# Performance work log

Measured on AMD Instinct MI355X. Metric: run time of the kernel, lower is better.

The kernel has to match this reference:

```python
import jax, jax.numpy as jnp
import numpy as np

EMBED_DIM = 256
B, H, S = 8, 20, 1024


def setup_inputs() -> dict:
    key = jax.random.key(0)
    ks = jax.random.split(key, 10)
    E = EMBED_DIM
    d2, d4 = 2 * E, 4 * E

    def lin(kw, kb, out_dim, in_dim):
        bound = 1.0 / np.sqrt(in_dim)
        w = jax.random.uniform(kw, (out_dim, in_dim), minval=-bound, maxval=bound, dtype=jnp.float32)
        b = jax.random.uniform(kb, (out_dim,), minval=-bound, maxval=bound, dtype=jnp.float32)
        return w, b

    wc_w, wc_b = lin(ks[0], ks[1], d2, d2)
    wh_w, wh_b = lin(ks[2], ks[3], d2, d2)
    qt_w, qt_b = lin(ks[4], ks[5], 1, d2)
    wf_w, wf_b = lin(ks[6], ks[7], E, d4)

    hist = jax.random.normal(ks[8], (B, H, S, d2), dtype=jnp.float32)
    cur = jax.random.normal(ks[9], (B, S, d2), dtype=jnp.float32)
    return {
        "wca_history_embeddings": hist,
        "wca_current_embeddings": cur,
        "wc_w": wc_w, "wc_b": wc_b,
        "wh_w": wh_w, "wh_b": wh_b,
        "qt_w": qt_w, "qt_b": qt_b,
        "wf_w": wf_w, "wf_b": wf_b,
    }


def reference(wca_history_embeddings, wca_current_embeddings,
              wc_w, wc_b, wh_w, wh_b, qt_w, qt_b, wf_w, wf_b):
    # hist: [B, H, S, 2E]; cur: [B, S, 2E]
    c_proj = jnp.einsum('bsd,ed->bse', wca_current_embeddings, wc_w) + wc_b   # [B,S,2E]
    h_proj = jnp.einsum('bhsd,ed->bhse', wca_history_embeddings, wh_w) + wh_b  # [B,H,S,2E]
    gate = jax.nn.sigmoid(c_proj[:, None, :, :] + h_proj)                      # [B,H,S,2E]
    # alpha[b,h,s] = qt(gate) -- raw scores, NO softmax (matches original)
    alpha = jnp.einsum('bhse,e->bhs', gate, qt_w[0]) + qt_b[0]                 # [B,H,S]
    # weighted neighbor sum over history dim
    summed = jnp.einsum('bhs,bhsd->bsd', alpha, wca_history_embeddings)        # [B,S,2E]
    fused = jnp.concatenate([wca_current_embeddings, summed], axis=-1)         # [B,S,4E]
    final = jnp.einsum('bsd,ed->bse', fused, wf_w) + wf_b                      # [B,S,E]
    return final
```

## Files before the change

### kernel.cpp

```cpp
#include <hip/hip_runtime.h>
#include <hip/hip_bf16.h>
#include <stdint.h>

static constexpr int Bn = 8, Hn = 20, Sn = 1024, En = 256, D2 = 512, D4 = 1024;
static constexpr int Mall = Bn * Hn * Sn;
static constexpr int BS   = Bn * Sn;

typedef __attribute__((ext_vector_type(8))) short bf16x8;
typedef __attribute__((ext_vector_type(4))) float f32x4;

__device__ __forceinline__ unsigned short f2bf(float f) {
  unsigned int u = __float_as_uint(f);
  u += 0x7FFFu + ((u >> 16) & 1u);
  return (unsigned short)(u >> 16);
}
__device__ __forceinline__ float bf2f(unsigned short u) {
  return __uint_as_float(((unsigned int)u) << 16);
}
__device__ __forceinline__ float sigmoid_fast(float x) {
  return __builtin_amdgcn_rcpf(1.0f + __expf(-x));
}
__device__ __forceinline__ unsigned int packbf_trunc(float a, float b) {
  return __builtin_amdgcn_perm(__float_as_uint(b), __float_as_uint(a),
                               0x07060302u);
}
__device__ __forceinline__ unsigned int packbf_rne(float a, float b) {
  return ((unsigned int)f2bf(b) << 16) | (unsigned int)f2bf(a);
}
__device__ __forceinline__ uint4 pack8_trunc(float4 f0, float4 f1) {
  uint4 p;
  p.x = packbf_trunc(f0.x, f0.y);
  p.y = packbf_trunc(f0.z, f0.w);
  p.z = packbf_trunc(f1.x, f1.y);
  p.w = packbf_trunc(f1.z, f1.w);
  return p;
}

typedef const __attribute__((address_space(1))) void gv_t;
typedef __attribute__((address_space(3))) void lv_t;
__device__ __forceinline__ void gload_lds16(const void* g, void* l) {
  __builtin_amdgcn_global_load_lds((gv_t*)g, (lv_t*)l, 16, 0, 0);
}

__global__ __launch_bounds__(256) void k_convert_weights(
    const float* __restrict__ wc, const float* __restrict__ wh,
    const float* __restrict__ wf,
    unsigned short* __restrict__ wcb, unsigned short* __restrict__ whb,
    unsigned short* __restrict__ wfb) {
  int idx4 = blockIdx.x * 256 + threadIdx.x;
  int a = idx4 >> 16;
  int r = idx4 & 65535;
  const float* s = (a == 0) ? wc : (a == 1) ? wh : wf;
  unsigned short* d = (a == 0) ? wcb : (a == 1) ? whb : wfb;
  float4 v = reinterpret_cast<const float4*>(s)[r];
  ushort4 o;
  o.x = f2bf(v.x); o.y = f2bf(v.y); o.z = f2bf(v.z); o.w = f2bf(v.w);
  reinterpret_cast<ushort4*>(d)[r] = o;
}

template <int MODE>
__global__ __launch_bounds__(256) void k_gemm_bt(
    const float* __restrict__ A,
    const unsigned short* __restrict__ Bw,
    const float* __restrict__ bias,
    const unsigned short* __restrict__ cproj,
    const float* __restrict__ qtw,
    const float* __restrict__ qtb,
    unsigned short* __restrict__ cproj_out,
    float* __restrict__ alpha_out) {
  __shared__ __align__(16) unsigned char ldsA[128 * 128];
  __shared__ __align__(16) unsigned char ldsB[128 * 128];

  const int tid = threadIdx.x;
  const int lane = tid & 63, wave = tid >> 6;
  const int lrow = lane & 15, lk = lane >> 4;
  const int row0 = blockIdx.x * 128;
  const f32x4 zero4 = {0.f, 0.f, 0.f, 0.f};

  float asum[2][4];
  if (MODE == 1) {
#pragma unroll
    for (int rf = 0; rf < 2; ++rf)
#pragma unroll
      for (int r = 0; r < 4; ++r) asum[rf][r] = 0.f;
  }

  const int nc_begin = (MODE == 0) ? blockIdx.y : 0;
  const int nc_end   = (MODE == 0) ? (int)blockIdx.y + 1 : 4;

  for (int nc = nc_begin; nc < nc_end; ++nc) {
    f32x4 acc[2][8];
#pragma unroll
    for (int rf = 0; rf < 2; ++rf)
#pragma unroll
      for (int cf = 0; cf < 8; ++cf) acc[rf][cf] = zero4;

    for (int kt = 0; kt < 8; ++kt) {
      __syncthreads();
#pragma unroll
      for (int slot = 0; slot < 4; ++slot) {
        int idx = (slot * 256 + tid) * 8;
        int row = idx >> 6, k = idx & 63;
        const float* src = A + (size_t)(row0 + row) * 512 + kt * 64 + k;
        float4 f0 = *reinterpret_cast<const float4*>(src);
        float4 f1 = *reinterpret_cast<const float4*>(src + 4);
        uint4 p = pack8_trunc(f0, f1);
        int off = row * 128 + ((k * 2) ^ ((row & 7) << 4));
        *reinterpret_cast<uint4*>(ldsA + off) = p;
      }
#pragma unroll
      for (int c = 0; c < 4; ++c) {
        int ci = c * 256 + tid;
        int n = ci >> 3, kc = (ci & 7) * 8;
        const unsigned short* src =
            Bw + (size_t)(nc * 128 + n) * 512 + kt * 64 + kc;
        uint4 p = *reinterpret_cast<const uint4*>(src);
        int off = n * 128 + ((kc * 2) ^ ((n & 7) << 4));
        *reinterpret_cast<uint4*>(ldsB + off) = p;
      }
      __syncthreads();
#pragma unroll
      for (int ks = 0; ks < 2; ++ks) {
        int kbyte = ks * 64 + lk * 16;
        bf16x8 af[2];
#pragma unroll
        for (int rf = 0; rf < 2; ++rf) {
          int ar = wave * 32 + rf * 16 + lrow;
          af[rf] = *reinterpret_cast<const bf16x8*>(
              ldsA + ar * 128 + (kbyte ^ ((ar & 7) << 4)));
        }
#pragma unroll
        for (int cf = 0; cf < 8; ++cf) {
          int br = cf * 16 + lrow;
          bf16x8 bf = *reinterpret_cast<const bf16x8*>(
              ldsB + br * 128 + (kbyte ^ ((br & 7) << 4)));
#pragma unroll
          for (int rf = 0; rf < 2; ++rf)
            acc[rf][cf] = __builtin_amdgcn_mfma_f32_16x16x32_bf16(
                af[rf], bf, acc[rf][cf], 0, 0, 0);
        }
      }
    }

    if (MODE == 0) {
#pragma unroll
      for (int cf = 0; cf < 8; ++cf) {
        int e = nc * 128 + cf * 16 + lrow;
        float bse = bias[e];
#pragma unroll
        for (int rf = 0; rf < 2; ++rf)
#pragma unroll
          for (int r = 0; r < 4; ++r) {
            int row = row0 + wave * 32 + rf * 16 + lk * 4 + r;
            cproj_out[(size_t)row * 512 + e] = f2bf(acc[rf][cf][r] + bse);
          }
      }
    } else {
#pragma unroll
      for (int cf = 0; cf < 8; ++cf) {
        int e = nc * 128 + cf * 16 + lrow;
        float whb = bias[e];
        float qw = qtw[e];
#pragma unroll
        for (int rf = 0; rf < 2; ++rf)
#pragma unroll
          for (int r = 0; r < 4; ++r) {
            int row = row0 + wave * 32 + rf * 16 + lk * 4 + r;
            int bsrow = ((row / (Hn * Sn)) << 10) | (row & 1023);
            float cp = bf2f(cproj[(size_t)bsrow * 512 + e]);
            float g = sigmoid_fast(acc[rf][cf][r] + whb + cp);
            asum[rf][r] = fmaf(g, qw, asum[rf][r]);
          }
      }
    }
  }

  if (MODE == 1) {
#pragma unroll
    for (int off = 1; off < 16; off <<= 1) {
#pragma unroll
      for (int rf = 0; rf < 2; ++rf)
#pragma unroll
        for (int r = 0; r < 4; ++r)
          asum[rf][r] += __shfl_xor(asum[rf][r], off, 64);
    }
    if (lrow == 0) {
      float qb = qtb[0];
#pragma unroll
      for (int rf = 0; rf < 2; ++rf)
#pragma unroll
        for (int r = 0; r < 4; ++r) {
          int row = row0 + wave * 32 + rf * 16 + lk * 4 + r;
          alpha_out[row] = asum[rf][r] + qb;
        }
    }
  }
}

__global__ __launch_bounds__(512, 2) void k_alpha_summed(
    const float* __restrict__ A,
    const unsigned short* __restrict__ Bw,
    const float* __restrict__ bias,
    const unsigned short* __restrict__ cproj,
    const float* __restrict__ qtw,
    const float* __restrict__ qtb,
    unsigned short* __restrict__ summed) {
  __shared__ __align__(16) unsigned char ldsA[81920];
  __shared__ __align__(16) unsigned char ldsB[65536];
  __shared__ __align__(16) unsigned char ldsC[4096];

  const int tid = threadIdx.x;
  const int lane = tid & 63, wave = tid >> 6;
  const int lrow = lane & 15, lk = lane >> 4;
  const int wc = wave;
  const int b = blockIdx.x >> 8;
  const int s0 = (blockIdx.x & 255) * 4;
  const size_t rowbase = (size_t)b * 20480;
  const f32x4 zero4 = {0.f, 0.f, 0.f, 0.f};

  const unsigned short* gB0 =
      Bw + (size_t)(wave * 64 + (lane >> 2)) * 512 +
      ((lane & 3) ^ ((lane >> 3) & 3)) * 8;

  auto issueB = [&](int k) {
#pragma unroll
    for (int j = 0; j < 4; ++j)
      gload_lds16(gB0 + (size_t)j * 8192 + k * 32,
                  (char*)ldsB + (k & 1) * 32768 + wave * 4096 + j * 1024);
  };

  float4 pa0[5], pa1[5];
  auto issueA = [&](int bt, float4 (&pa)[5]) {
#pragma unroll
    for (int j = 0; j < 5; ++j) {
      int u = (bt * 5 + j) * 512 + tid;
      int mr = u >> 7, c4 = u & 127;
      pa[j] = *reinterpret_cast<const float4*>(
          A + (rowbase + (size_t)(mr >> 2) * 1024 + s0 + (mr & 3)) * 512 +
          c4 * 4);
    }
  };
  auto writeA = [&](int bt, float4 (&pa)[5]) {
#pragma unroll
    for (int j = 0; j < 5; ++j) {
      int u = (bt * 5 + j) * 512 + tid;
      int mr = u >> 7, c4 = u & 127;
      unsigned int u0 = packbf_rne(pa[j].x, pa[j].y);
      unsigned int u1 = packbf_rne(pa[j].z, pa[j].w);
      int off = mr * 1024 + (((c4 >> 1) ^ (mr & 7)) << 4) + ((c4 & 1) << 3);
      *reinterpret_cast<uint2*>(ldsA + off) = make_uint2(u0, u1);
    }
  };

  if (wave < 4) {
    const unsigned short* csrc = cproj + ((size_t)b * 1024 + s0) * 512;
    gload_lds16(csrc + tid * 8, (char*)ldsC + wave * 1024);
  }
  issueA(0, pa0);
  issueA(1, pa1);
  writeA(0, pa0);
  issueA(2, pa0);
  writeA(1, pa1);
  issueA(3, pa1);
  writeA(2, pa0);
  writeA(3, pa1);
  issueB(0);
  issueB(1);
  __syncthreads();

  f32x4 acc[5][4];
#pragma unroll
  for (int tm = 0; tm < 5; ++tm)
#pragma unroll
    for (int n = 0; n < 4; ++n) acc[tm][n] = zero4;

#pragma unroll 4
  for (int k = 0; k < 16; ++k) {
    bf16x8 af[5];
#pragma unroll
    for (int tm = 0; tm < 5; ++tm) {
      int r = tm * 16 + lrow;
      int g = (k * 4 + lk) ^ (r & 7);
      af[tm] = *reinterpret_cast<const bf16x8*>(ldsA + r * 1024 + g * 16);
    }
    const unsigned char* bbase = ldsB + (k & 1) * 32768 + wave * 4096;
#pragma unroll
    for (int n = 0; n < 4; ++n) {
      int rl = n * 16 + lrow;
      int slot = lk ^ ((rl >> 1) & 3);
      bf16x8 bv = *reinterpret_cast<const bf16x8*>(bbase + rl * 64 + slot * 16);
#pragma unroll
      for (int tm = 0; tm < 5; ++tm)
        acc[tm][n] = __builtin_amdgcn_mfma_f32_16x16x32_bf16(af[tm], bv,
                                                             acc[tm][n], 0, 0,
                                                             0);
    }
    asm volatile("s_waitcnt lgkmcnt(0)" ::: "memory");
    __builtin_amdgcn_sched_barrier(0);
    if (k < 14) {
      issueB(k + 2);
      __builtin_amdgcn_sched_barrier(0);
      asm volatile("s_waitcnt vmcnt(4)" ::: "memory");
    } else if (k == 14) {
      asm volatile("s_waitcnt vmcnt(0)" ::: "memory");
    }
    __builtin_amdgcn_sched_barrier(0);
  }

  float asum[5][4];
#pragma unroll
  for (int tm = 0; tm < 5; ++tm)
#pragma unroll
    for (int r = 0; r < 4; ++r) asum[tm][r] = 0.f;

  const unsigned short* cpl = reinterpret_cast<const unsigned short*>(ldsC);
#pragma unroll
  for (int n = 0; n < 4; ++n) {
    int e = wc * 64 + n * 16 + lrow;
    float whb = bias[e];
    float qw = qtw[e];
    float cpv[4];
#pragma unroll
    for (int si = 0; si < 4; ++si) cpv[si] = bf2f(cpl[si * 512 + e]);
#pragma unroll
    for (int tm = 0; tm < 5; ++tm)
#pragma unroll
      for (int r = 0; r < 4; ++r) {
        float g = sigmoid_fast(acc[tm][n][r] + whb + cpv[r]);
        asum[tm][r] = fmaf(g, qw, asum[tm][r]);
      }
  }
#pragma unroll
  for (int off = 1; off < 16; off <<= 1)
#pragma unroll
    for (int tm = 0; tm < 5; ++tm)
#pragma unroll
      for (int r = 0; r < 4; ++r)
        asum[tm][r] += __shfl_xor(asum[tm][r], off, 64);

  __syncthreads();
  float* red = reinterpret_cast<float*>(ldsB);
  if (lrow == 0) {
#pragma unroll
    for (int tm = 0; tm < 5; ++tm)
#pragma unroll
      for (int r = 0; r < 4; ++r)
        red[wc * 80 + tm * 16 + lk * 4 + r] = asum[tm][r];
  }
  __syncthreads();

  if (wave < 4) {
    const int si = wave;
    const float qb = qtb[0];
    float o[8];
#pragma unroll
    for (int j = 0; j < 8; ++j) o[j] = 0.f;
#pragma unroll
    for (int h = 0; h < 20; ++h) {
      int mr = h * 4 + si;
      float a = qb;
#pragma unroll
      for (int wq = 0; wq < 8; ++wq) a += red[wq * 80 + mr];
      int g = lane ^ (mr & 7);
      bf16x8 av = *reinterpret_cast<const bf16x8*>(ldsA + mr * 1024 + g * 16);
#pragma unroll
      for (int j = 0; j < 8; ++j)
        o[j] = fmaf(a, bf2f((unsigned short)av[j]), o[j]);
    }
    uint4 pk;
    pk.x = packbf_rne(o[0], o[1]);
    pk.y = packbf_rne(o[2], o[3]);
    pk.z = packbf_rne(o[4], o[5]);
    pk.w = packbf_rne(o[6], o[7]);
    size_t orow = (size_t)b * 1024 + s0 + si;
    reinterpret_cast<uint4*>(summed)[orow * 64 + lane] = pk;
  }
}

__global__ __launch_bounds__(256) void k_summed(
    const float* __restrict__ hist, const float* __restrict__ alpha,
    unsigned short* __restrict__ summed) {
  int idx = blockIdx.x * 256 + threadIdx.x;
  int bs = idx >> 7, c4 = idx & 127;
  int b = bs >> 10, s = bs & 1023;
  const float4* hp = reinterpret_cast<const float4*>(hist);
  float4 acc = make_float4(0.f, 0.f, 0.f, 0.f);
#pragma unroll
  for (int h = 0; h < Hn; ++h) {
    int bh = b * Hn + h;
    float a = alpha[(bh << 10) + s];
    float4 v = hp[(size_t)(bh * 1024 + s) * 128 + c4];
    acc.x = fmaf(a, v.x, acc.x);
    acc.y = fmaf(a, v.y, acc.y);
    acc.z = fmaf(a, v.z, acc.z);
    acc.w = fmaf(a, v.w, acc.w);
  }
  ushort4 o;
  o.x = f2bf(acc.x); o.y = f2bf(acc.y); o.z = f2bf(acc.z); o.w = f2bf(acc.w);
  reinterpret_cast<ushort4*>(summed)[idx] = o;
}

__global__ __launch_bounds__(256) void k_final(
    const float* __restrict__ cur,
    const unsigned short* __restrict__ summed,
    const unsigned short* __restrict__ wfb16,
    const float* __restrict__ wf_bias,
    float* __restrict__ out) {
  __shared__ __align__(16) unsigned char ldsA[64 * 128];
  __shared__ __align__(16) unsigned char ldsB[128 * 128];
  const int tid = threadIdx.x;
  const int lane = tid & 63, wave = tid >> 6;
  const int lrow = lane & 15, lk = lane >> 4;
  const int row0 = blockIdx.x * 64;
  const int n0 = blockIdx.y * 128;
  const f32x4 zero4 = {0.f, 0.f, 0.f, 0.f};

  f32x4 acc[8];
#pragma unroll
  for (int cf = 0; cf < 8; ++cf) acc[cf] = zero4;

  for (int kt = 0; kt < 16; ++kt) {
    __syncthreads();
#pragma unroll
    for (int slot = 0; slot < 2; ++slot) {
      int idx = (slot * 256 + tid) * 8;
      int row = idx >> 6, k = idx & 63;
      int gcol = kt * 64 + k;
      uint4 p;
      if (kt < 8) {
        const float* src = cur + (size_t)(row0 + row) * 512 + gcol;
        float4 f0 = *reinterpret_cast<const float4*>(src);
        float4 f1 = *reinterpret_cast<const float4*>(src + 4);
        p = pack8_trunc(f0, f1);
      } else {
        p = *reinterpret_cast<const uint4*>(
            summed + (size_t)(row0 + row) * 512 + gcol - 512);
      }
      int off = row * 128 + ((k * 2) ^ ((row & 7) << 4));
      *reinterpret_cast<uint4*>(ldsA + off) = p;
    }
#pragma unroll
    for (int c = 0; c < 4; ++c) {
      int ci = c * 256 + tid;
      int n = ci >> 3, kc = (ci & 7) * 8;
      uint4 p = *reinterpret_cast<const uint4*>(
          wfb16 + (size_t)(n0 + n) * 1024 + kt * 64 + kc);
      int off = n * 128 + ((kc * 2) ^ ((n & 7) << 4));
      *reinterpret_cast<uint4*>(ldsB + off) = p;
    }
    __syncthreads();
#pragma unroll
    for (int ks = 0; ks < 2; ++ks) {
      int kbyte = ks * 64 + lk * 16;
      int ar = wave * 16 + lrow;
      bf16x8 a = *reinterpret_cast<const bf16x8*>(
          ldsA + ar * 128 + (kbyte ^ ((ar & 7) << 4)));
#pragma unroll
      for (int cf = 0; cf < 8; ++cf) {
        int br = cf * 16 + lrow;
        bf16x8 b = *reinterpret_cast<const bf16x8*>(
            ldsB + br * 128 + (kbyte ^ ((br & 7) << 4)));
        acc[cf] = __builtin_amdgcn_mfma_f32_16x16x32_bf16(a, b, acc[cf], 0, 0, 0);
      }
    }
  }
#pragma unroll
  for (int cf = 0; cf < 8; ++cf) {
    int col = n0 + cf * 16 + lrow;
    float bse = wf_bias[col];
#pragma unroll
    for (int r = 0; r < 4; ++r) {
      int row = row0 + wave * 16 + lk * 4 + r;
      out[(size_t)row * 256 + col] = acc[cf][r] + bse;
    }
  }
}

extern "C" void kernel_launch(void* const* d_in, const int* in_sizes, int n_in,
                              void* d_out, int out_size, void* d_ws,
                              size_t ws_size, hipStream_t stream) {
  (void)in_sizes; (void)n_in; (void)out_size;
  const float* hist = (const float*)d_in[0];
  const float* cur  = (const float*)d_in[1];
  const float* wc_w = (const float*)d_in[2];
  const float* wc_b = (const float*)d_in[3];
  const float* wh_w = (const float*)d_in[4];
  const float* wh_b = (const float*)d_in[5];
  const float* qt_w = (const float*)d_in[6];
  const float* qt_b = (const float*)d_in[7];
  const float* wf_w = (const float*)d_in[8];
  const float* wf_b = (const float*)d_in[9];
  float* out = (float*)d_out;
  char* ws = (char*)d_ws;

  unsigned short* wcb    = (unsigned short*)(ws);
  unsigned short* whb    = (unsigned short*)(ws + 524288);
  unsigned short* wfb    = (unsigned short*)(ws + 1048576);
  unsigned short* cproj  = (unsigned short*)(ws + 1572864);
  float*          alpha  = (float*)(ws + 9961472);
  unsigned short* summed = (unsigned short*)(ws + 10616832);
  const size_t NEED = 19005440;

  k_convert_weights<<<dim3(768), dim3(256), 0, stream>>>(wc_w, wh_w, wf_w, wcb,
                                                         whb, wfb);
  k_gemm_bt<0><<<dim3(BS / 128, 4), dim3(256), 0, stream>>>(
      cur, wcb, wc_b, nullptr, nullptr, nullptr, cproj, nullptr);
  if (ws_size >= NEED) {
    k_alpha_summed<<<dim3(2048), dim3(512), 0, stream>>>(
        hist, whb, wh_b, cproj, qt_w, qt_b, summed);
  } else {
    k_gemm_bt<1><<<dim3(Mall / 128, 1), dim3(256), 0, stream>>>(
        hist, whb, wh_b, cproj, qt_w, qt_b, nullptr, alpha);
    k_summed<<<dim3(4096), dim3(256), 0, stream>>>(hist, alpha, summed);
  }
  k_final<<<dim3(BS / 64, 2), dim3(256), 0, stream>>>(cur, summed, wfb, wf_b,
                                                      out);
}
```

Baseline: 223.0 us.

## Halve per-block sequence tile in fused alpha kernel to raise occupancy

Each block of the fused alpha/summed kernel now covers 2 sequence positions (40 history rows, padded to 3 M-tiles) instead of 4. This shrinks LDS use and raises the launch-bounds occupancy target, and the grid grows to 4096 blocks. The c_proj staging buffer is dropped in favour of direct global loads. B-weight loading changes from double-buffered async prefetch to a single buffer guarded by __syncthreads each k-step. The aim is more resident blocks to hide memory latency, but each weight tile is now reloaded for half as many rows, padding wastes some MFMA work, and load/compute overlap is reduced.

New measurement: 257.0 us. +15.3%, slower.

```diff
diff --git a/kernel.cpp b/kernel.cpp
--- a/kernel.cpp
+++ b/kernel.cpp
@@ -197,7 +197,7 @@
   }
 }
 
-__global__ __launch_bounds__(512, 2) void k_alpha_summed(
+__global__ __launch_bounds__(512, 4) void k_alpha_summed(
     const float* __restrict__ A,
     const unsigned short* __restrict__ Bw,
     const float* __restrict__ bias,
@@ -205,28 +205,26 @@
     const float* __restrict__ qtw,
     const float* __restrict__ qtb,
     unsigned short* __restrict__ summed) {
-  __shared__ __align__(16) unsigned char ldsA[81920];
-  __shared__ __align__(16) unsigned char ldsB[65536];
-  __shared__ __align__(16) unsigned char ldsC[4096];
+  __shared__ __align__(16) unsigned char ldsA[49152];
+  __shared__ __align__(16) unsigned char ldsB[32768];
 
   const int tid = threadIdx.x;
   const int lane = tid & 63, wave = tid >> 6;
   const int lrow = lane & 15, lk = lane >> 4;
   const int wc = wave;
-  const int b = blockIdx.x >> 8;
-  const int s0 = (blockIdx.x & 255) * 4;
+  const int b = blockIdx.x >> 9;
+  const int s0 = (blockIdx.x & 511) * 2;
   const size_t rowbase = (size_t)b * 20480;
   const f32x4 zero4 = {0.f, 0.f, 0.f, 0.f};
 
   const unsigned short* gB0 =
-      Bw + (size_t)(wave * 64 + (lane >> 2)) * 512 +
-      ((lane & 3) ^ ((lane >> 3) & 3)) * 8;
-
+      Bw + (size_t)(lane >> 2) * 512 + ((lane & 3) ^ ((lane >> 3) & 3)) * 8;
   auto issueB = [&](int k) {
 #pragma unroll
-    for (int j = 0; j < 4; ++j)
-      gload_lds16(gB0 + (size_t)j * 8192 + k * 32,
-                  (char*)ldsB + (k & 1) * 32768 + wave * 4096 + j * 1024);
+    for (int j = 0; j < 4; ++j) {
+      int W = j * 8 + wave;
+      gload_lds16(gB0 + (size_t)W * 8192 + k * 32, (char*)ldsB + W * 1024);
+    }
   };
 
   float4 pa0[5], pa1[5];
@@ -236,7 +234,7 @@
       int u = (bt * 5 + j) * 512 + tid;
       int mr = u >> 7, c4 = u & 127;
       pa[j] = *reinterpret_cast<const float4*>(
-          A + (rowbase + (size_t)(mr >> 2) * 1024 + s0 + (mr & 3)) * 512 +
+          A + (rowbase + (size_t)(mr >> 1) * 1024 + s0 + (mr & 1)) * 512 +
           c4 * 4);
     }
   };
@@ -245,111 +243,93 @@
     for (int j = 0; j < 5; ++j) {
       int u = (bt * 5 + j) * 512 + tid;
       int mr = u >> 7, c4 = u & 127;
-      unsigned int u0 = packbf_rne(pa[j].x, pa[j].y);
-      unsigned int u1 = packbf_rne(pa[j].z, pa[j].w);
       int off = mr * 1024 + (((c4 >> 1) ^ (mr & 7)) << 4) + ((c4 & 1) << 3);
-      *reinterpret_cast<uint2*>(ldsA + off) = make_uint2(u0, u1);
+      *reinterpret_cast<uint2*>(ldsA + off) =
+          make_uint2(packbf_rne(pa[j].x, pa[j].y),
+                     packbf_rne(pa[j].z, pa[j].w));
     }
   };
 
-  if (wave < 4) {
-    const unsigned short* csrc = cproj + ((size_t)b * 1024 + s0) * 512;
-    gload_lds16(csrc + tid * 8, (char*)ldsC + wave * 1024);
-  }
   issueA(0, pa0);
   issueA(1, pa1);
   writeA(0, pa0);
-  issueA(2, pa0);
   writeA(1, pa1);
-  issueA(3, pa1);
-  writeA(2, pa0);
-  writeA(3, pa1);
   issueB(0);
-  issueB(1);
   __syncthreads();
 
-  f32x4 acc[5][4];
-#pragma unroll
-  for (int tm = 0; tm < 5; ++tm)
+  f32x4 acc[3][4];
+#pragma unroll
+  for (int tm = 0; tm < 3; ++tm)
 #pragma unroll
     for (int n = 0; n < 4; ++n) acc[tm][n] = zero4;
 
-#pragma unroll 4
   for (int k = 0; k < 16; ++k) {
-    bf16x8 af[5];
-#pragma unroll
-    for (int tm = 0; tm < 5; ++tm) {
+    bf16x8 af[3];
+#pragma unroll
+    for (int tm = 0; tm < 3; ++tm) {
       int r = tm * 16 + lrow;
       int g = (k * 4 + lk) ^ (r & 7);
       af[tm] = *reinterpret_cast<const bf16x8*>(ldsA + r * 1024 + g * 16);
     }
-    const unsigned char* bbase = ldsB + (k & 1) * 32768 + wave * 4096;
 #pragma unroll
     for (int n = 0; n < 4; ++n) {
-      int rl = n * 16 + lrow;
+      int rl = wc * 64 + n * 16 + lrow;
       int slot = lk ^ ((rl >> 1) & 3);
-      bf16x8 bv = *reinterpret_cast<const bf16x8*>(bbase + rl * 64 + slot * 16);
-#pragma unroll
-      for (int tm = 0; tm < 5; ++tm)
+      bf16x8 bv = *reinterpret_cast<const bf16x8*>(ldsB + rl * 64 + slot * 16);
+#pragma unroll
+      for (int tm = 0; tm < 3; ++tm)
         acc[tm][n] = __builtin_amdgcn_mfma_f32_16x16x32_bf16(af[tm], bv,
                                                              acc[tm][n], 0, 0,
                                                              0);
     }
-    asm volatile("s_waitcnt lgkmcnt(0)" ::: "memory");
-    __builtin_amdgcn_sched_barrier(0);
-    if (k < 14) {
-      issueB(k + 2);
-      __builtin_amdgcn_sched_barrier(0);
-      asm volatile("s_waitcnt vmcnt(4)" ::: "memory");
-    } else if (k == 14) {
-      asm volatile("s_waitcnt vmcnt(0)" ::: "memory");
-    }
-    __builtin_amdgcn_sched_barrier(0);
-  }
-
-  float asum[5][4];
-#pragma unroll
-  for (int tm = 0; tm < 5; ++tm)
+    __syncthreads();
+    if (k < 15) {
+      issueB(k + 1);
+      __syncthreads();
+    }
+  }
+
+  float asum[3][4];
+#pragma unroll
+  for (int tm = 0; tm < 3; ++tm)
 #pragma unroll
     for (int r = 0; r < 4; ++r) asum[tm][r] = 0.f;
 
-  const unsigned short* cpl = reinterpret_cast<const unsigned short*>(ldsC);
+  const size_t cpbase = ((size_t)b * 1024 + s0) * 512;
 #pragma unroll
   for (int n = 0; n < 4; ++n) {
     int e = wc * 64 + n * 16 + lrow;
     float whb = bias[e];
     float qw = qtw[e];
-    float cpv[4];
-#pragma unroll
-    for (int si = 0; si < 4; ++si) cpv[si] = bf2f(cpl[si * 512 + e]);
-#pragma unroll
-    for (int tm = 0; tm < 5; ++tm)
+    float cp0 = bf2f(cproj[cpbase + e]);
+    float cp1 = bf2f(cproj[cpbase + 512 + e]);
+#pragma unroll
+    for (int tm = 0; tm < 3; ++tm)
 #pragma unroll
       for (int r = 0; r < 4; ++r) {
-        float g = sigmoid_fast(acc[tm][n][r] + whb + cpv[r]);
+        float g = sigmoid_fast(acc[tm][n][r] + whb + ((r & 1) ? cp1 : cp0));
         asum[tm][r] = fmaf(g, qw, asum[tm][r]);
       }
   }
 #pragma unroll
   for (int off = 1; off < 16; off <<= 1)
 #pragma unroll
-    for (int tm = 0; tm < 5; ++tm)
+    for (int tm = 0; tm < 3; ++tm)
 #pragma unroll
       for (int r = 0; r < 4; ++r)
         asum[tm][r] += __shfl_xor(asum[tm][r], off, 64);
 
-  __syncthreads();
   float* red = reinterpret_cast<float*>(ldsB);
   if (lrow == 0) {
 #pragma unroll
-    for (int tm = 0; tm < 5; ++tm)
+    for (int tm = 0; tm < 3; ++tm)
 #pragma unroll
       for (int r = 0; r < 4; ++r)
-        red[wc * 80 + tm * 16 + lk * 4 + r] = asum[tm][r];
+        red[wc * 48 + tm * 16 + lk * 4 + r] = asum[tm][r];
   }
   __syncthreads();
 
-  if (wave < 4) {
+  if (wave < 2) {
     const int si = wave;
     const float qb = qtb[0];
     float o[8];
@@ -357,10 +337,10 @@
     for (int j = 0; j < 8; ++j) o[j] = 0.f;
 #pragma unroll
     for (int h = 0; h < 20; ++h) {
-      int mr = h * 4 + si;
+      int mr = h * 2 + si;
       float a = qb;
 #pragma unroll
-      for (int wq = 0; wq < 8; ++wq) a += red[wq * 80 + mr];
+      for (int w = 0; w < 8; ++w) a += red[w * 48 + mr];
       int g = lane ^ (mr & 7);
       bf16x8 av = *reinterpret_cast<const bf16x8*>(ldsA + mr * 1024 + g * 16);
 #pragma unroll
@@ -506,7 +486,7 @@
   k_gemm_bt<0><<<dim3(BS / 128, 4), dim3(256), 0, stream>>>(
       cur, wcb, wc_b, nullptr, nullptr, nullptr, cproj, nullptr);
   if (ws_size >= NEED) {
-    k_alpha_summed<<<dim3(2048), dim3(512), 0, stream>>>(
+    k_alpha_summed<<<dim3(4096), dim3(512), 0, stream>>>(
         hist, whb, wh_b, cproj, qt_w, qt_b, summed);
   } else {
     k_gemm_bt<1><<<dim3(Mall / 128, 1), dim3(256), 0, stream>>>(
```

## Load weight fragments directly into registers instead of staging through LDS

Applied to the files above, without the earlier changes.

In the fused alpha/summed kernel, the weight (B) operand is now read straight from global memory into registers with a three-deep register prefetch ring, in place of the double-buffered LDS staging with explicit waitcnt barriers. This removes 64KB of LDS per block and the LDS write/read traffic for B. The K loop is fully unrolled through a macro, and the reduction buffer moves to a small dedicated LDS array, which also drops one __syncthreads. The trade-offs are higher register pressure from the prefetch ring and global load latency that is now hidden only by a short prefetch distance.

Result: slower. 260.9 us (+17.0%).

```diff
diff --git a/kernel.cpp b/kernel.cpp
--- a/kernel.cpp
+++ b/kernel.cpp
@@ -206,8 +206,8 @@
     const float* __restrict__ qtb,
     unsigned short* __restrict__ summed) {
   __shared__ __align__(16) unsigned char ldsA[81920];
-  __shared__ __align__(16) unsigned char ldsB[65536];
   __shared__ __align__(16) unsigned char ldsC[4096];
+  __shared__ float ldsR[8 * 80];
 
   const int tid = threadIdx.x;
   const int lane = tid & 63, wave = tid >> 6;
@@ -218,15 +218,17 @@
   const size_t rowbase = (size_t)b * 20480;
   const f32x4 zero4 = {0.f, 0.f, 0.f, 0.f};
 
-  const unsigned short* gB0 =
-      Bw + (size_t)(wave * 64 + (lane >> 2)) * 512 +
-      ((lane & 3) ^ ((lane >> 3) & 3)) * 8;
-
-  auto issueB = [&](int k) {
-#pragma unroll
-    for (int j = 0; j < 4; ++j)
-      gload_lds16(gB0 + (size_t)j * 8192 + k * 32,
-                  (char*)ldsB + (k & 1) * 32768 + wave * 4096 + j * 1024);
+  const char* gB = reinterpret_cast<const char*>(Bw);
+  int boff[4];
+#pragma unroll
+  for (int n = 0; n < 4; ++n)
+    boff[n] = ((wc * 64 + n * 16 + lrow) << 10) + (lk << 4);
+
+  bf16x8 bv0[4], bv1[4], bv2[4];
+  auto loadB = [&](int K, bf16x8 (&bv)[4]) {
+#pragma unroll
+    for (int n = 0; n < 4; ++n)
+      bv[n] = *reinterpret_cast<const bf16x8*>(gB + boff[n] + K * 64);
   };
 
   float4 pa0[5], pa1[5];
@@ -264,8 +266,6 @@
   issueA(3, pa1);
   writeA(2, pa0);
   writeA(3, pa1);
-  issueB(0);
-  issueB(1);
   __syncthreads();
 
   f32x4 acc[5][4];
@@ -274,38 +274,33 @@
 #pragma unroll
     for (int n = 0; n < 4; ++n) acc[tm][n] = zero4;
 
-#pragma unroll 4
-  for (int k = 0; k < 16; ++k) {
-    bf16x8 af[5];
-#pragma unroll
-    for (int tm = 0; tm < 5; ++tm) {
-      int r = tm * 16 + lrow;
-      int g = (k * 4 + lk) ^ (r & 7);
-      af[tm] = *reinterpret_cast<const bf16x8*>(ldsA + r * 1024 + g * 16);
-    }
-    const unsigned char* bbase = ldsB + (k & 1) * 32768 + wave * 4096;
-#pragma unroll
-    for (int n = 0; n < 4; ++n) {
-      int rl = n * 16 + lrow;
-      int slot = lk ^ ((rl >> 1) & 3);
-      bf16x8 bv = *reinterpret_cast<const bf16x8*>(bbase + rl * 64 + slot * 16);
-#pragma unroll
-      for (int tm = 0; tm < 5; ++tm)
-        acc[tm][n] = __builtin_amdgcn_mfma_f32_16x16x32_bf16(af[tm], bv,
-                                                             acc[tm][n], 0, 0,
-                                                             0);
-    }
-    asm volatile("s_waitcnt lgkmcnt(0)" ::: "memory");
-    __builtin_amdgcn_sched_barrier(0);
-    if (k < 14) {
-      issueB(k + 2);
-      __builtin_amdgcn_sched_barrier(0);
-      asm volatile("s_waitcnt vmcnt(4)" ::: "memory");
-    } else if (k == 14) {
-      asm volatile("s_waitcnt vmcnt(0)" ::: "memory");
-    }
-    __builtin_amdgcn_sched_barrier(0);
-  }
+  loadB(0, bv0);
+  loadB(1, bv1);
+  loadB(2, bv2);
+
+#define KSTEP(K, BV)                                                       \
+  {                                                                        \
+    bf16x8 af[5];                                                          \
+    _Pragma("unroll") for (int tm = 0; tm < 5; ++tm) {                     \
+      int r = tm * 16 + lrow;                                              \
+      int g = ((K) * 4 + lk) ^ (r & 7);                                    \
+      af[tm] =                                                             \
+          *reinterpret_cast<const bf16x8*>(ldsA + r * 1024 + g * 16);      \
+    }                                                                      \
+    _Pragma("unroll") for (int n = 0; n < 4; ++n)                          \
+        _Pragma("unroll") for (int tm = 0; tm < 5; ++tm) acc[tm][n] =      \
+        __builtin_amdgcn_mfma_f32_16x16x32_bf16(af[tm], BV[n],             \
+                                                acc[tm][n], 0, 0, 0);      \
+    if ((K) < 13) loadB((K) + 3, BV);                                      \
+  }
+
+  KSTEP(0, bv0)  KSTEP(1, bv1)  KSTEP(2, bv2)
+  KSTEP(3, bv0)  KSTEP(4, bv1)  KSTEP(5, bv2)
+  KSTEP(6, bv0)  KSTEP(7, bv1)  KSTEP(8, bv2)
+  KSTEP(9, bv0)  KSTEP(10, bv1) KSTEP(11, bv2)
+  KSTEP(12, bv0) KSTEP(13, bv1) KSTEP(14, bv2)
+  KSTEP(15, bv0)
+#undef KSTEP
 
   float asum[5][4];
 #pragma unroll
@@ -338,14 +333,12 @@
       for (int r = 0; r < 4; ++r)
         asum[tm][r] += __shfl_xor(asum[tm][r], off, 64);
 
-  __syncthreads();
-  float* red = reinterpret_cast<float*>(ldsB);
   if (lrow == 0) {
 #pragma unroll
     for (int tm = 0; tm < 5; ++tm)
 #pragma unroll
       for (int r = 0; r < 4; ++r)
-        red[wc * 80 + tm * 16 + lk * 4 + r] = asum[tm][r];
+        ldsR[wc * 80 + tm * 16 + lk * 4 + r] = asum[tm][r];
   }
   __syncthreads();
 
@@ -360,7 +353,7 @@
       int mr = h * 4 + si;
       float a = qb;
 #pragma unroll
-      for (int wq = 0; wq < 8; ++wq) a += red[wq * 80 + mr];
+      for (int wq = 0; wq < 8; ++wq) a += ldsR[wq * 80 + mr];
       int g = lane ^ (mr & 7);
       bf16x8 av = *reinterpret_cast<const bf16x8*>(ldsA + mr * 1024 + g * 16);
 #pragma unroll
```
